# Kernel tuning notes

Hardware: AMD Instinct MI355X
Metric: run time of the kernel (lower is better)

## Reference

```python
import jax, jax.numpy as jnp
import numpy as np
from jax import lax

RATES = (2, 3, 5, 9)
C_IN = 64
B, H, W = 4, 128, 128


def conv2d(x, w, b, dilation):
    # x: [B,C,H,W], w: [O,I,3,3]; padding=dilation keeps spatial size
    y = lax.conv_general_dilated(
        x, w, window_strides=(1, 1),
        padding=[(dilation, dilation), (dilation, dilation)],
        rhs_dilation=(dilation, dilation),
        dimension_numbers=('NCHW', 'OIHW', 'NCHW'))
    return y + b[None, :, None, None]


def bilinear_sample(x, py, px):
    # x: [B,C,H,W]; py,px: [B,K,H,W] float sampling positions; zeros outside
    Hh, Ww = x.shape[-2], x.shape[-1]
    y0 = jnp.floor(py)
    x0 = jnp.floor(px)
    wy1 = py - y0
    wx1 = px - x0
    wy0 = 1.0 - wy1
    wx0 = 1.0 - wx1

    def gather(yi, xi):
        valid = (yi >= 0) & (yi < Hh) & (xi >= 0) & (xi < Ww)
        yc = jnp.clip(yi, 0, Hh - 1).astype(jnp.int32)
        xc = jnp.clip(xi, 0, Ww - 1).astype(jnp.int32)
        # per-batch fancy gather: [C,K,H,W]
        vals = jax.vmap(lambda im, yy, xx: im[:, yy, xx])(x, yc, xc)
        return vals * valid[:, None].astype(x.dtype)

    out = (gather(y0, x0) * (wy0 * wx0)[:, None]
           + gather(y0, x0 + 1) * (wy0 * wx1)[:, None]
           + gather(y0 + 1, x0) * (wy1 * wx0)[:, None]
           + gather(y0 + 1, x0 + 1) * (wy1 * wx1)[:, None])
    return out  # [B,C,K,H,W]


def deform_conv(x, offset, weight, dilation):
    # offset: [B,18,H,W] = (dy,dx) per kernel point; weight: [O,C,3,3]
    b, c, h, w = x.shape
    K = 9
    off = offset.reshape(b, K, 2, h, w)
    dy, dx = off[:, :, 0], off[:, :, 1]
    ky = jnp.repeat((jnp.arange(3) - 1) * dilation, 3).astype(x.dtype)  # [9]
    kx = jnp.tile((jnp.arange(3) - 1) * dilation, 3).astype(x.dtype)
    hh = jnp.arange(h, dtype=x.dtype)[None, None, :, None]
    ww = jnp.arange(w, dtype=x.dtype)[None, None, None, :]
    py = hh + ky[None, :, None, None] + dy
    px = ww + kx[None, :, None, None] + dx
    sampled = bilinear_sample(x, py, px)  # [B,C,K,H,W]
    w9 = weight.reshape(weight.shape[0], c, K)
    return jnp.einsum('bckhw,ock->bohw', sampled, w9)


def setup_inputs() -> dict:
    key = jax.random.key(0)
    ks = jax.random.split(key, 8)
    s = 0.05
    return {
        'x': jax.random.normal(ks[0], (B, C_IN, H, W), jnp.float32),
        'dw': jax.random.normal(ks[1], (4, C_IN, C_IN, 3, 3), jnp.float32) * s,
        'ow': jax.random.normal(ks[2], (4, 18, C_IN, 3, 3), jnp.float32) * s,
        'ob': jax.random.normal(ks[3], (4, 18), jnp.float32) * s,
        'se_w1': jax.random.normal(ks[4], (C_IN, 4 * C_IN), jnp.float32) * s,
        'se_b1': jax.random.normal(ks[5], (C_IN,), jnp.float32) * s,
        'se_w2': jax.random.normal(ks[6], (4 * C_IN, C_IN), jnp.float32) * s,
        'se_b2': jax.random.normal(ks[7], (4 * C_IN,), jnp.float32) * s,
    }


def reference(x, dw, ow, ob, se_w1, se_b1, se_w2, se_b2):
    b, c, h, w = x.shape
    outs = []
    for i in range(4):
        j = (i - 1) % 4  # faithful to `self.offsets[i - 1]` in the source
        off = jax.nn.relu(conv2d(x, ow[j], ob[j], RATES[j]))
        outs.append(deform_conv(x, off, dw[i], RATES[i]))
    cat = jnp.concatenate(outs, axis=1)  # [B,4C,H,W]
    # SENet on concatenated features
    g = cat.mean(axis=(2, 3))  # [B,4C]
    h1 = jax.nn.relu(g @ se_w1.T + se_b1)
    s = jax.nn.sigmoid(h1 @ se_w2.T + se_b2)  # [B,4C]
    gated = (1.0 + s)[:, :, None, None] * cat
    fused = gated.reshape(b, 4, c, h, w).sum(axis=1)  # sum over the 4 stages
    return x + fused
```

## Files before the change

### kernel.cpp

```cpp
#include <hip/hip_runtime.h>
#include <hip/hip_bf16.h>
#include <math.h>

#define BATCH 4
#define CIN 64
#define HH 128
#define WW 128
#define HWP (HH*WW)

#define OFF_OFF   0
#define CAT_OFF   4718592
#define XBF_OFF   (CAT_OFF + 8388608)
#define XHWC_OFF  (XBF_OFF + 2097152)
#define WTB_OFF   (CAT_OFF + 16777216)
#define OWT_OFF   (WTB_OFF + 147456)
#define G_OFF     (OWT_OFF + 41472)
#define SCALE_OFF (G_OFF + 1024)

typedef __attribute__((ext_vector_type(8))) short short8;
typedef __attribute__((ext_vector_type(8))) unsigned short ushort8;
typedef __attribute__((ext_vector_type(4))) float f32x4;

__device__ __forceinline__ int rate_of(int i) {
    return (i == 0) ? 2 : (i == 1) ? 3 : (i == 2) ? 5 : 9;
}

__device__ __forceinline__ short f2bf(float f) {
    union { float f; unsigned u; } v; v.f = f;
    unsigned u = v.u + 0x7FFFu + ((v.u >> 16) & 1u);
    return (short)(u >> 16);
}
__device__ __forceinline__ float bf2f(unsigned short u) {
    union { unsigned u; float f; } v; v.u = ((unsigned)u) << 16;
    return v.f;
}

__global__ __launch_bounds__(256) void prep_kernel(
    const float* __restrict__ x,  const float* __restrict__ dw,
    const float* __restrict__ ow, unsigned short* __restrict__ xbf,
    short* __restrict__ wtb, float* __restrict__ owT)
{
    int idx = blockIdx.x * 256 + threadIdx.x;
    if (idx < 4194304) {
        xbf[idx] = (unsigned short)f2bf(x[idx]);
        return;
    }
    int idx1 = idx - 4194304;
    if (idx1 < 147456) {
        int c = idx1 & 63;
        int k = (idx1 >> 6) % 9;
        int r = idx1 / 576;
        int o = r & 63;
        int i = r >> 6;
        wtb[idx1] = f2bf(dw[((i * 64 + o) * 64 + c) * 9 + k]);
        return;
    }
    int idx2 = idx1 - 147456;
    if (idx2 < 41472) {
        int o = idx2 % 18;
        int r = idx2 / 18;
        int tap = r % 9; r /= 9;
        int c = r & 63;
        int j = r >> 6;
        owT[idx2] = ow[((j * 18 + o) * 64 + c) * 9 + tap];
    }
}

__global__ __launch_bounds__(256) void xhwc_kernel(
    const float* __restrict__ x, unsigned short* __restrict__ xhwc)
{
    const int t  = threadIdx.x;
    const int b  = blockIdx.y;
    const int p0 = blockIdx.x * 64;
    const int px = t & 63;
    const int cO = t >> 6;

    const float* xb = x + (size_t)b * CIN * HWP + p0 + px;
    unsigned short* xh = xhwc + ((size_t)b * HWP + p0 + px) * 64;

#pragma unroll
    for (int g = 0; g < 2; ++g) {
        const int cb = cO * 8 + g * 32;
        ushort8 v;
#pragma unroll
        for (int cj = 0; cj < 8; ++cj)
            v[cj] = (unsigned short)f2bf(xb[(size_t)(cb + cj) * HWP]);
        *(ushort8*)(xh + cb) = v;
    }
}

__global__ __launch_bounds__(256) void offset_conv_kernel(
    const unsigned short* __restrict__ xbf, const float* __restrict__ owT,
    const float* __restrict__ ob, float* __restrict__ off)
{
    const int t  = threadIdx.x;
    const int lx = t & 63, ly = t >> 6;
    const int w0 = blockIdx.x * 64 + lx;
    const int h0 = blockIdx.y * 4 + ly;
    const int z  = blockIdx.z;
    const int j  = z >> 2, b = z & 3;
    const int d  = rate_of(j);

    int addr[9]; float msk[9];
#pragma unroll
    for (int tap = 0; tap < 9; ++tap) {
        const int iy = tap / 3, ix = tap % 3;
        const int xx = w0 + (ix - 1) * d;
        const int yy = h0 + (iy - 1) * d;
        const bool v = ((unsigned)xx < (unsigned)WW) && ((unsigned)yy < (unsigned)HH);
        addr[tap] = min(max(yy, 0), HH - 1) * WW + min(max(xx, 0), WW - 1);
        msk[tap]  = v ? 1.f : 0.f;
    }

    float acc[18];
#pragma unroll
    for (int o = 0; o < 18; ++o) acc[o] = ob[j * 18 + o];

    const unsigned short* xb = xbf + (size_t)b * CIN * HWP;
    float p[9];
#pragma unroll
    for (int tap = 0; tap < 9; ++tap) p[tap] = bf2f(xb[addr[tap]]);

    for (int c = 0; c < CIN; ++c) {
        const unsigned short* xn = xb + (c < CIN - 1 ? c + 1 : CIN - 1) * HWP;
        float q[9];
#pragma unroll
        for (int tap = 0; tap < 9; ++tap) q[tap] = bf2f(xn[addr[tap]]);

        const float* wp = owT + ((j * 64 + c) * 9) * 18;
#pragma unroll
        for (int tap = 0; tap < 9; ++tap) {
            const float v = p[tap] * msk[tap];
            const float* wt = wp + tap * 18;
#pragma unroll
            for (int o = 0; o < 18; ++o)
                acc[o] = fmaf(v, wt[o], acc[o]);
        }
#pragma unroll
        for (int tap = 0; tap < 9; ++tap) p[tap] = q[tap];
    }

    float* op = off + (size_t)z * 18 * HWP + h0 * WW + w0;
#pragma unroll
    for (int o = 0; o < 18; ++o) op[o * HWP] = fmaxf(acc[o], 0.f);
}

__global__ __launch_bounds__(256) void deform_mfma_kernel(
    const unsigned short* __restrict__ xhwc, const short* __restrict__ wtb,
    const float* __restrict__ off, unsigned short* __restrict__ cat)
{
    __shared__ __align__(16) short S[128][72];

    const int t  = threadIdx.x;
    const int z  = blockIdx.y;
    const int i  = z >> 2, b = z & 3;
    const int d  = rate_of(i);
    const int j  = (i + 3) & 3;
    const int ty = blockIdx.x >> 1;
    const int tx = blockIdx.x & 1;

    const int chunk = t & 7;
    const int pxb   = t >> 3;

    const int wv = t >> 6, lane = t & 63;
    const int nl = lane & 15, quad = lane >> 4;

    const unsigned short* xh = xhwc + (size_t)b * HWP * 64;
    const float* offb = off + ((size_t)(j * 4 + b) * 18) * HWP;

    f32x4 acc[8];
#pragma unroll
    for (int a = 0; a < 8; ++a) acc[a] = (f32x4){0.f, 0.f, 0.f, 0.f};

    for (int k = 0; k < 9; ++k) {
        const int iy = k / 3, ix = k % 3;

        if (k) __syncthreads();

#pragma unroll
        for (int it = 0; it < 4; ++it) {
            const int psub = it * 32 + pxb;
            const int sly = psub >> 6, slx = psub & 63;
            const int ph = ty * 2 + sly, pw = tx * 64 + slx;
            const int pg = ph * WW + pw;

            float dy = offb[(2 * k) * HWP + pg];
            float dx = offb[(2 * k + 1) * HWP + pg];
            float py = (float)(ph + (iy - 1) * d) + dy;
            float px = (float)(pw + (ix - 1) * d) + dx;
            float fy0 = floorf(py), fx0 = floorf(px);
            float wy1 = py - fy0, wx1 = px - fx0;
            float wy0 = 1.f - wy1, wx0 = 1.f - wx1;
            int y0 = (int)fy0, x0 = (int)fx0;
            int y1 = y0 + 1,  x1 = x0 + 1;
            bool vy0 = (unsigned)y0 < (unsigned)HH, vy1 = (unsigned)y1 < (unsigned)HH;
            bool vx0 = (unsigned)x0 < (unsigned)WW, vx1 = (unsigned)x1 < (unsigned)WW;
            int yc0 = min(max(y0, 0), HH - 1), yc1 = min(max(y1, 0), HH - 1);
            int xc0 = min(max(x0, 0), WW - 1), xc1 = min(max(x1, 0), WW - 1);
            float w00 = (vy0 && vx0) ? wy0 * wx0 : 0.f;
            float w01 = (vy0 && vx1) ? wy0 * wx1 : 0.f;
            float w10 = (vy1 && vx0) ? wy1 * wx0 : 0.f;
            float w11 = (vy1 && vx1) ? wy1 * wx1 : 0.f;

            const int cb = chunk * 8;
            ushort8 u00 = *(const ushort8*)(xh + (size_t)(yc0 * WW + xc0) * 64 + cb);
            ushort8 u01 = *(const ushort8*)(xh + (size_t)(yc0 * WW + xc1) * 64 + cb);
            ushort8 u10 = *(const ushort8*)(xh + (size_t)(yc1 * WW + xc0) * 64 + cb);
            ushort8 u11 = *(const ushort8*)(xh + (size_t)(yc1 * WW + xc1) * 64 + cb);

            short8 pk;
#pragma unroll
            for (int cj = 0; cj < 8; ++cj) {
                float v = bf2f(u00[cj]) * w00 + bf2f(u01[cj]) * w01
                        + bf2f(u10[cj]) * w10 + bf2f(u11[cj]) * w11;
                pk[cj] = f2bf(v);
            }
            *(__shared__ short8*)&S[psub][cb] = pk;
        }
        __syncthreads();

#pragma unroll
        for (int q2 = 0; q2 < 2; ++q2) {
            short8 b0 = *(const __shared__ short8*)&S[wv * 32 + nl][q2 * 32 + quad * 8];
            short8 b1 = *(const __shared__ short8*)&S[wv * 32 + 16 + nl][q2 * 32 + quad * 8];
#pragma unroll
            for (int mt = 0; mt < 4; ++mt) {
                const short* wrow = wtb
                    + ((size_t)((i * 64 + mt * 16 + nl) * 9 + k)) * 64;
                short8 a = *(const short8*)&wrow[q2 * 32 + quad * 8];
                acc[mt * 2 + 0] = __builtin_amdgcn_mfma_f32_16x16x32_bf16(a, b0, acc[mt * 2 + 0], 0, 0, 0);
                acc[mt * 2 + 1] = __builtin_amdgcn_mfma_f32_16x16x32_bf16(a, b1, acc[mt * 2 + 1], 0, 0, 0);
            }
        }
    }

#pragma unroll
    for (int mt = 0; mt < 4; ++mt) {
#pragma unroll
        for (int nt = 0; nt < 2; ++nt) {
            const int psub = wv * 32 + nt * 16 + nl;
            const int prow = ty * 2 + (psub >> 6);
            const int pcol = tx * 64 + (psub & 63);
            unsigned short* cp = cat
                + ((size_t)(b * 256 + i * 64 + mt * 16 + quad * 4)) * HWP
                + prow * WW + pcol;
            const f32x4 v = acc[mt * 2 + nt];
#pragma unroll
            for (int r = 0; r < 4; ++r)
                cp[(size_t)r * HWP] = (unsigned short)f2bf(v[r]);
        }
    }
}

__global__ __launch_bounds__(256) void reduce_kernel(
    const unsigned short* __restrict__ cat, float* __restrict__ g)
{
    const int bc = blockIdx.x;
    const unsigned short* p = cat + (size_t)bc * HWP;
    float s = 0.f;
#pragma unroll
    for (int q = 0; q < 8; ++q) {
        short8 v8 = *(const short8*)(p + q * 2048 + threadIdx.x * 8);
#pragma unroll
        for (int e = 0; e < 8; ++e) s += bf2f((unsigned short)v8[e]);
    }
#pragma unroll
    for (int o = 32; o > 0; o >>= 1) s += __shfl_down(s, o, 64);
    __shared__ float ls[4];
    if ((threadIdx.x & 63) == 0) ls[threadIdx.x >> 6] = s;
    __syncthreads();
    if (threadIdx.x == 0) {
        g[bc] = (ls[0] + ls[1] + ls[2] + ls[3]) * (1.f / (float)HWP);
    }
}

__global__ __launch_bounds__(256) void se_kernel(
    const float* __restrict__ g,  const float* __restrict__ w1,
    const float* __restrict__ b1, const float* __restrict__ w2,
    const float* __restrict__ b2, float* __restrict__ scale)
{
    __shared__ float gs[1024];
    __shared__ float h1s[256];
    const int t = threadIdx.x;
#pragma unroll
    for (int q = 0; q < 4; ++q) gs[q * 256 + t] = g[q * 256 + t];
    __syncthreads();
    {
        int b = t >> 6, o = t & 63;
        float a = b1[o];
        for (int c = 0; c < 256; ++c)
            a = fmaf(gs[b * 256 + c], w1[o * 256 + c], a);
        h1s[t] = fmaxf(a, 0.f);
    }
    __syncthreads();
#pragma unroll
    for (int q = 0; q < 4; ++q) {
        int idx = q * 256 + t;
        int b = idx >> 8, cc = idx & 255;
        float a = b2[cc];
#pragma unroll 8
        for (int o = 0; o < 64; ++o)
            a = fmaf(h1s[b * 64 + o], w2[cc * 64 + o], a);
        scale[idx] = 1.f + 1.f / (1.f + expf(-a));
    }
}

__global__ __launch_bounds__(256) void final_kernel(
    const float* __restrict__ x, const unsigned short* __restrict__ cat,
    const float* __restrict__ scale, float* __restrict__ out)
{
    const int gid = blockIdx.x;
    const int p = (gid & 63) * 256 + threadIdx.x;
    const int c = (gid >> 6) & 63;
    const int b = gid >> 12;
    const float s0 = scale[b * 256 + c];
    const float s1 = scale[b * 256 + 64 + c];
    const float s2 = scale[b * 256 + 128 + c];
    const float s3 = scale[b * 256 + 192 + c];
    const unsigned short* cb = cat + ((size_t)(b * 256 + c)) * HWP + p;
    float v = x[(size_t)(b * 64 + c) * HWP + p];
    v = fmaf(s0, bf2f(cb[0 * 64 * HWP]), v);
    v = fmaf(s1, bf2f(cb[1 * 64 * HWP]), v);
    v = fmaf(s2, bf2f(cb[2 * 64 * HWP]), v);
    v = fmaf(s3, bf2f(cb[3 * 64 * HWP]), v);
    out[(size_t)(b * 64 + c) * HWP + p] = v;
}

extern "C" void kernel_launch(void* const* d_in, const int* in_sizes, int n_in,
                              void* d_out, int out_size, void* d_ws, size_t ws_size,
                              hipStream_t stream) {
    const float* x  = (const float*)d_in[0];
    const float* dw = (const float*)d_in[1];
    const float* ow = (const float*)d_in[2];
    const float* ob = (const float*)d_in[3];
    const float* w1 = (const float*)d_in[4];
    const float* b1 = (const float*)d_in[5];
    const float* w2 = (const float*)d_in[6];
    const float* b2 = (const float*)d_in[7];
    float* out = (float*)d_out;
    float* ws  = (float*)d_ws;

    float* OFF            = ws + OFF_OFF;
    unsigned short* CAT   = (unsigned short*)(ws + CAT_OFF);
    unsigned short* XBF   = (unsigned short*)(ws + XBF_OFF);
    unsigned short* XHWC  = (unsigned short*)(ws + XHWC_OFF);
    short* WTB            = (short*)(ws + WTB_OFF);
    float* OWT            = ws + OWT_OFF;
    float* G              = ws + G_OFF;
    float* SCALE          = ws + SCALE_OFF;

    prep_kernel<<<17122, 256, 0, stream>>>(x, dw, ow, XBF, WTB, OWT);
    xhwc_kernel<<<dim3(256, 4), 256, 0, stream>>>(x, XHWC);
    offset_conv_kernel<<<dim3(2, 32, 16), 256, 0, stream>>>(XBF, OWT, ob, OFF);
    deform_mfma_kernel<<<dim3(128, 16), 256, 0, stream>>>(XHWC, WTB, OFF, CAT);
    reduce_kernel<<<1024, 256, 0, stream>>>(CAT, G);
    se_kernel<<<1, 256, 0, stream>>>(G, w1, b1, w2, b2, SCALE);
    final_kernel<<<16384, 256, 0, stream>>>(x, CAT, SCALE, out);
}
```

Measured before the change: 342.1 us.

## Move offset convolution to bf16 MFMA using channels-last input; drop NCHW bf16 copy

The scalar FMA offset convolution, which read a planar bf16 copy of x, is replaced by an MFMA kernel. It stages 64-pixel channels-last tiles per tap in shared memory and multiplies them against bf16 offset weights padded from 18 to 32 outputs. The prep kernel no longer converts all of x to planar bf16 and instead packs the offset weights in bf16, which removes a large conversion pass and its workspace buffer. The cost is bf16 offset weights and wasted MFMA lanes on the padded output rows. Two shared-memory pointer casts in the deform kernel are also simplified.

```diff
diff --git a/kernel.cpp b/kernel.cpp
--- a/kernel.cpp
+++ b/kernel.cpp
@@ -10,11 +10,10 @@
 
 #define OFF_OFF   0
 #define CAT_OFF   4718592
-#define XBF_OFF   (CAT_OFF + 8388608)
-#define XHWC_OFF  (XBF_OFF + 2097152)
-#define WTB_OFF   (CAT_OFF + 16777216)
-#define OWT_OFF   (WTB_OFF + 147456)
-#define G_OFF     (OWT_OFF + 41472)
+#define XHWC_OFF  (CAT_OFF + 8388608)
+#define WTB_OFF   (XHWC_OFF + 2097152)
+#define OWB_OFF   (WTB_OFF + 73728)
+#define G_OFF     (OWB_OFF + 36864)
 #define SCALE_OFF (G_OFF + 1024)
 
 typedef __attribute__((ext_vector_type(8))) short short8;
@@ -36,33 +35,29 @@
 }
 
 __global__ __launch_bounds__(256) void prep_kernel(
-    const float* __restrict__ x,  const float* __restrict__ dw,
-    const float* __restrict__ ow, unsigned short* __restrict__ xbf,
-    short* __restrict__ wtb, float* __restrict__ owT)
+    const float* __restrict__ dw, const float* __restrict__ ow,
+    short* __restrict__ wtb, short* __restrict__ owb)
 {
     int idx = blockIdx.x * 256 + threadIdx.x;
-    if (idx < 4194304) {
-        xbf[idx] = (unsigned short)f2bf(x[idx]);
-        return;
-    }
-    int idx1 = idx - 4194304;
-    if (idx1 < 147456) {
-        int c = idx1 & 63;
-        int k = (idx1 >> 6) % 9;
-        int r = idx1 / 576;
+    if (idx < 147456) {
+        int c = idx & 63;
+        int k = (idx >> 6) % 9;
+        int r = idx / 576;
         int o = r & 63;
         int i = r >> 6;
-        wtb[idx1] = f2bf(dw[((i * 64 + o) * 64 + c) * 9 + k]);
+        wtb[idx] = f2bf(dw[((i * 64 + o) * 64 + c) * 9 + k]);
         return;
     }
-    int idx2 = idx1 - 147456;
-    if (idx2 < 41472) {
-        int o = idx2 % 18;
-        int r = idx2 / 18;
-        int tap = r % 9; r /= 9;
-        int c = r & 63;
-        int j = r >> 6;
-        owT[idx2] = ow[((j * 18 + o) * 64 + c) * 9 + tap];
+    int idx2 = idx - 147456;
+    if (idx2 < 73728) {
+        int c = idx2 & 63;
+        int r = idx2 >> 6;
+        int o = r & 31;
+        int r2 = r >> 5;
+        int tap = r2 % 9;
+        int j = r2 / 9;
+        owb[idx2] = (o < 18) ? f2bf(ow[((j * 18 + o) * 64 + c) * 9 + tap])
+                             : (short)0;
     }
 }
 
@@ -89,60 +84,74 @@
     }
 }
 
-__global__ __launch_bounds__(256) void offset_conv_kernel(
-    const unsigned short* __restrict__ xbf, const float* __restrict__ owT,
+__global__ __launch_bounds__(256) void offset_mfma_kernel(
+    const unsigned short* __restrict__ xhwc, const short* __restrict__ owb,
     const float* __restrict__ ob, float* __restrict__ off)
 {
+    __shared__ __align__(16) short S2[64][72];
+
     const int t  = threadIdx.x;
-    const int lx = t & 63, ly = t >> 6;
-    const int w0 = blockIdx.x * 64 + lx;
-    const int h0 = blockIdx.y * 4 + ly;
-    const int z  = blockIdx.z;
+    const int z  = blockIdx.y;
     const int j  = z >> 2, b = z & 3;
     const int d  = rate_of(j);
-
-    int addr[9]; float msk[9];
-#pragma unroll
-    for (int tap = 0; tap < 9; ++tap) {
-        const int iy = tap / 3, ix = tap % 3;
-        const int xx = w0 + (ix - 1) * d;
-        const int yy = h0 + (iy - 1) * d;
-        const bool v = ((unsigned)xx < (unsigned)WW) && ((unsigned)yy < (unsigned)HH);
-        addr[tap] = min(max(yy, 0), HH - 1) * WW + min(max(xx, 0), WW - 1);
-        msk[tap]  = v ? 1.f : 0.f;
-    }
-
-    float acc[18];
-#pragma unroll
-    for (int o = 0; o < 18; ++o) acc[o] = ob[j * 18 + o];
-
-    const unsigned short* xb = xbf + (size_t)b * CIN * HWP;
-    float p[9];
-#pragma unroll
-    for (int tap = 0; tap < 9; ++tap) p[tap] = bf2f(xb[addr[tap]]);
-
-    for (int c = 0; c < CIN; ++c) {
-        const unsigned short* xn = xb + (c < CIN - 1 ? c + 1 : CIN - 1) * HWP;
-        float q[9];
-#pragma unroll
-        for (int tap = 0; tap < 9; ++tap) q[tap] = bf2f(xn[addr[tap]]);
-
-        const float* wp = owT + ((j * 64 + c) * 9) * 18;
-#pragma unroll
-        for (int tap = 0; tap < 9; ++tap) {
-            const float v = p[tap] * msk[tap];
-            const float* wt = wp + tap * 18;
-#pragma unroll
-            for (int o = 0; o < 18; ++o)
-                acc[o] = fmaf(v, wt[o], acc[o]);
-        }
-#pragma unroll
-        for (int tap = 0; tap < 9; ++tap) p[tap] = q[tap];
-    }
-
-    float* op = off + (size_t)z * 18 * HWP + h0 * WW + w0;
-#pragma unroll
-    for (int o = 0; o < 18; ++o) op[o * HWP] = fmaxf(acc[o], 0.f);
+    const int p0 = blockIdx.x * 64;
+    const int ph = p0 >> 7;
+    const int cb0 = p0 & 127;
+
+    const int wv = t >> 6, lane = t & 63;
+    const int nl = lane & 15, quad = lane >> 4;
+
+    const unsigned short* xh = xhwc + (size_t)b * HWP * 64;
+
+    f32x4 acc[2];
+    acc[0] = (f32x4){0.f, 0.f, 0.f, 0.f};
+    acc[1] = (f32x4){0.f, 0.f, 0.f, 0.f};
+
+    for (int k = 0; k < 9; ++k) {
+        const int iy = k / 3, ix = k % 3;
+        const int ys = ph + (iy - 1) * d;
+        const bool rowok = (unsigned)ys < (unsigned)HH;
+
+        if (k) __syncthreads();
+
+#pragma unroll
+        for (int q = 0; q < 2; ++q) {
+            const int task = q * 256 + t;
+            const int px = task >> 3, chunk = task & 7;
+            const int xs = cb0 + px + (ix - 1) * d;
+            short8 v = {};
+            if (rowok && (unsigned)xs < (unsigned)WW)
+                v = *(const short8*)(xh + ((size_t)(ys * WW + xs)) * 64 + chunk * 8);
+            *(short8*)&S2[px][chunk * 8] = v;
+        }
+        __syncthreads();
+
+#pragma unroll
+        for (int q2 = 0; q2 < 2; ++q2) {
+            short8 a = *(const short8*)&S2[wv * 16 + nl][q2 * 32 + quad * 8];
+#pragma unroll
+            for (int nt = 0; nt < 2; ++nt) {
+                const short* brow = owb
+                    + ((size_t)((j * 9 + k) * 32 + nt * 16 + nl)) * 64;
+                short8 bf = *(const short8*)&brow[q2 * 32 + quad * 8];
+                acc[nt] = __builtin_amdgcn_mfma_f32_16x16x32_bf16(a, bf, acc[nt], 0, 0, 0);
+            }
+        }
+    }
+
+    float* op = off + (size_t)z * 18 * HWP + p0;
+#pragma unroll
+    for (int nt = 0; nt < 2; ++nt) {
+        const int o = nt * 16 + nl;
+        if (o < 18) {
+            const float bias = ob[j * 18 + o];
+#pragma unroll
+            for (int r = 0; r < 4; ++r) {
+                const int pxl = wv * 16 + quad * 4 + r;
+                op[(size_t)o * HWP + pxl] = fmaxf(acc[nt][r] + bias, 0.f);
+            }
+        }
+    }
 }
 
 __global__ __launch_bounds__(256) void deform_mfma_kernel(
@@ -215,14 +224,14 @@
                         + bf2f(u10[cj]) * w10 + bf2f(u11[cj]) * w11;
                 pk[cj] = f2bf(v);
             }
-            *(__shared__ short8*)&S[psub][cb] = pk;
+            *(short8*)&S[psub][cb] = pk;
         }
         __syncthreads();
 
 #pragma unroll
         for (int q2 = 0; q2 < 2; ++q2) {
-            short8 b0 = *(const __shared__ short8*)&S[wv * 32 + nl][q2 * 32 + quad * 8];
-            short8 b1 = *(const __shared__ short8*)&S[wv * 32 + 16 + nl][q2 * 32 + quad * 8];
+            short8 b0 = *(const short8*)&S[wv * 32 + nl][q2 * 32 + quad * 8];
+            short8 b1 = *(const short8*)&S[wv * 32 + 16 + nl][q2 * 32 + quad * 8];
 #pragma unroll
             for (int mt = 0; mt < 4; ++mt) {
                 const short* wrow = wtb
@@ -342,16 +351,15 @@
 
     float* OFF            = ws + OFF_OFF;
     unsigned short* CAT   = (unsigned short*)(ws + CAT_OFF);
-    unsigned short* XBF   = (unsigned short*)(ws + XBF_OFF);
     unsigned short* XHWC  = (unsigned short*)(ws + XHWC_OFF);
     short* WTB            = (short*)(ws + WTB_OFF);
-    float* OWT            = ws + OWT_OFF;
+    short* OWB            = (short*)(ws + OWB_OFF);
     float* G              = ws + G_OFF;
     float* SCALE          = ws + SCALE_OFF;
 
-    prep_kernel<<<17122, 256, 0, stream>>>(x, dw, ow, XBF, WTB, OWT);
+    prep_kernel<<<864, 256, 0, stream>>>(dw, ow, WTB, OWB);
     xhwc_kernel<<<dim3(256, 4), 256, 0, stream>>>(x, XHWC);
-    offset_conv_kernel<<<dim3(2, 32, 16), 256, 0, stream>>>(XBF, OWT, ob, OFF);
+    offset_mfma_kernel<<<dim3(256, 16), 256, 0, stream>>>(XHWC, OWB, ob, OFF);
     deform_mfma_kernel<<<dim3(128, 16), 256, 0, stream>>>(XHWC, WTB, OFF, CAT);
     reduce_kernel<<<1024, 256, 0, stream>>>(CAT, G);
     se_kernel<<<1, 256, 0, stream>>>(G, w1, b1, w2, b2, SCALE);
```

Result: faster. 326.3 us (-4.6%).
